# Kernel tuning notes

Measured on AMD Instinct MI355X. Metric: run time of the kernel, lower is better.

The kernel has to match this reference:

```python
import jax, jax.numpy as jnp
import numpy as np

VOC, EDIM, HDIM, SSZ, SDIM, SDEPTH, PAD = 32000, 256, 256, 128, 128, 2, 0
N, BSZ = 64, 32
T = 2 * N - 1  # 127
N_ACTS = 2  # push, pop


def _linear(key, out_d, in_d):
    k1, k2 = jax.random.split(key)
    return (jax.random.normal(k1, (out_d, in_d), jnp.float32) * 0.02,
            jax.random.normal(k2, (out_d,), jnp.float32) * 0.02)


def setup_inputs() -> dict:
    key = jax.random.key(0)
    ks = jax.random.split(key, 9)
    emb_W = jax.random.normal(ks[0], (VOC, EDIM), jnp.float32) * 0.02
    emb_W = emb_W.at[PAD].set(0.0)  # padding_idx row is zero in torch
    W_e2h, b_e2h = _linear(ks[1], HDIM, EDIM)
    W_s2h, b_s2h = _linear(ks[2], HDIM, SDIM * SDEPTH)
    W_h2h, b_h2h = _linear(ks[3], HDIM, HDIM)
    W_h2i, b_h2i = _linear(ks[4], N_ACTS + 1, HDIM)
    W_h2s, b_h2s = _linear(ks[5], SDIM, HDIM)
    W_s2u, b_s2u = _linear(ks[6], SDIM, SDIM * SDEPTH)
    empty_elem = jax.random.normal(ks[7], (1, SDIM), jnp.float32) * 0.02
    inputs = jax.random.randint(ks[8], (N, BSZ), 0, VOC)
    return dict(inputs=inputs, emb_W=emb_W, W_e2h=W_e2h, b_e2h=b_e2h,
                W_s2h=W_s2h, b_s2h=b_s2h, W_h2h=W_h2h, b_h2h=b_h2h,
                W_h2i=W_h2i, b_h2i=b_h2i, W_h2s=W_h2s, b_h2s=b_h2s,
                W_s2u=W_s2u, b_s2u=b_s2u, empty_elem=empty_elem)


def _srnn(inputs, emb_W, W_e2h, b_e2h, W_s2h, b_s2h, W_h2h, b_h2h,
          W_h2i, b_h2i, W_h2s, b_h2s, W_s2u, b_s2u, empty_elem):
    bsz = inputs.shape[1]
    embs = emb_W[inputs]                                        # [N, bsz, edim]
    pads = jnp.broadcast_to(emb_W[PAD], (T - N, bsz, EDIM))     # padded tail
    buf0 = jnp.concatenate([embs, pads], axis=0)                # [T, bsz, edim]
    hid0 = jnp.zeros((bsz, HDIM), jnp.float32)
    stack0 = jnp.broadcast_to(empty_elem, (bsz, SSZ, SDIM))

    def step(carry, t):
        hid, stack, buf = carry
        tops = stack[:, :SDEPTH, :].reshape(bsz, SDEPTH * SDIM)
        inp = buf[t]                                            # [bsz, edim]
        ihid = inp @ W_e2h.T + b_e2h + tops @ W_s2h.T + b_s2h
        hid = jax.nn.relu(hid @ W_h2h.T + b_h2h + ihid)
        inst = ihid @ W_h2i.T + b_h2i                           # [bsz, 3]
        act = jax.nn.softmax(inst[:, :N_ACTS], axis=-1)
        gamma = 1.0 + jnp.log1p(jnp.exp(inst[:, N_ACTS:]))      # [bsz, 1]
        a = act ** gamma
        a = a / (jnp.sum(a, axis=-1, keepdims=True) + 1e-16)    # sharpened acts
        p_push, p_pop = a[:, :1], a[:, 1:]                      # [bsz, 1]
        # buffer update: pop shifts the whole buffer down one slot along time
        buf_pop = jnp.concatenate([jnp.zeros_like(buf[:1]), buf[:-1]], axis=0)
        buf = p_push[None] * buf + p_pop[None] * buf_pop        # [1,bsz,1] bcast
        push_val = jax.nn.relu(hid @ W_h2s.T + b_h2s)           # [bsz, sdim]
        u_val = jax.nn.relu(tops @ W_s2u.T + b_s2u)             # [bsz, sdim]
        z = jnp.zeros((bsz, 1, SDIM), jnp.float32)
        # W_push (shift down by 1) as an index roll
        stack_push = jnp.concatenate([z, stack[:, :-1, :]], axis=1)
        stack_push = stack_push.at[:, 0, :].add(push_val)
        # W_pop = shift up by SDEPTH, then W_push = shift down by 1
        up = jnp.concatenate([stack[:, SDEPTH:, :],
                              jnp.zeros((bsz, SDEPTH, SDIM), jnp.float32)], axis=1)
        stack_pop = jnp.concatenate([z, up[:, :-1, :]], axis=1)
        stack_pop = stack_pop.at[:, 0, :].add(u_val)
        stack_pop = stack_pop.at[:, SSZ - SDEPTH + 1:, :].add(empty_elem[0])
        stack = p_push[:, :, None] * stack_push + p_pop[:, :, None] * stack_pop
        return (hid, stack, buf), (hid, a, stack[:, 0, :])

    (hid, stack, _), (outputs, acts, top_elems) = jax.lax.scan(
        step, (hid0, stack0, buf0), jnp.arange(T))
    return outputs, hid, stack, acts, top_elems


def reference(inputs, emb_W, W_e2h, b_e2h, W_s2h, b_s2h, W_h2h, b_h2h,
              W_h2i, b_h2i, W_h2s, b_h2s, W_s2u, b_s2u, empty_elem):
    return _srnn(inputs, emb_W, W_e2h, b_e2h, W_s2h, b_s2h, W_h2h, b_h2h,
                 W_h2i, b_h2i, W_h2s, b_h2s, W_s2u, b_s2u, empty_elem)
```

## Files before the change

kernel.cpp:

```cpp
#include <hip/hip_runtime.h>
#include <stdint.h>
#include <math.h>


#define T_STEPS 127

#define OUT_OFF   0
#define HID_OFF   1040384
#define STACK_OFF 1048576
#define ACTS_OFF  1572864
#define TE_OFF    1580992

#define WB_OFF 16384
#define E2H_OFF_U 131072

typedef _Float16 h2 __attribute__((ext_vector_type(2)));

__device__ __forceinline__ unsigned packh2(float a, float b){
  h2 v; v.x = (_Float16)a; v.y = (_Float16)b;
  return __builtin_bit_cast(unsigned, v);
}
__device__ __forceinline__ float h2loF(unsigned u){ h2 v = __builtin_bit_cast(h2,u); return (float)v.x; }
__device__ __forceinline__ float h2hiF(unsigned u){ h2 v = __builtin_bit_cast(h2,u); return (float)v.y; }

#if __has_builtin(__builtin_amdgcn_fdot2)
__device__ __forceinline__ float fdot2(unsigned a, unsigned b, float c){
  return __builtin_amdgcn_fdot2(__builtin_bit_cast(h2,a), __builtin_bit_cast(h2,b), c, false);
}
#else
__device__ __forceinline__ float fdot2(unsigned a, unsigned b, float c){
  return c + h2loF(a)*h2loF(b) + h2hiF(a)*h2hiF(b);
}
#endif

#if __has_builtin(__builtin_amdgcn_exp2f)
#define EXP2F(x) __builtin_amdgcn_exp2f(x)
#else
#define EXP2F(x) exp2f(x)
#endif
#if __has_builtin(__builtin_amdgcn_logf)
#define LOG2F(x) __builtin_amdgcn_logf(x)
#else
#define LOG2F(x) log2f(x)
#endif
#if __has_builtin(__builtin_amdgcn_rcpf)
#define RCPF(x) __builtin_amdgcn_rcpf(x)
#else
#define RCPF(x) (1.f/(x))
#endif

#define DPP_XOR1 0xB1
#define DPP_XOR2 0x4E
#define DPP_HM   0x141
#define DPP_RM   0x140
template<int CTRL>
__device__ __forceinline__ float dppadd(float v){
  int s = __builtin_amdgcn_update_dpp(0, __builtin_bit_cast(int, v), CTRL, 0xF, 0xF, true);
  return v + __builtin_bit_cast(float, s);
}

#define BAR() asm volatile("s_waitcnt lgkmcnt(0)\n\ts_barrier" ::: "memory")

#define CHOFF(u) (12*((u)>>3) + ((u)&7))

__global__ void prep_all(const int* __restrict__ inputs, const float* __restrict__ embW,
                         const float* __restrict__ We2h,
                         const float* __restrict__ Ws2h, const float* __restrict__ Wh2h,
                         const float* __restrict__ Wh2s, const float* __restrict__ Ws2u,
                         uint4* __restrict__ out4, unsigned* __restrict__ e2hpk){
  int tid = threadIdx.x;
  int bi  = blockIdx.x;
  if (bi >= 256){
    int gid = (bi-256)*256 + tid;
    const float* src;
    if (gid < 16384){
      int i = gid >> 10, t_ = gid & 1023;
      const float* S = (t_ < 512) ? Ws2h : Wh2h;
      int r = t_ & 511, jp = r >> 2, ks = r & 3;
      int j = 2*jp + (i >> 3);
      int k0 = ks*64 + (i & 7)*8;
      src = S + j*256 + k0;
    } else {
      int l = gid - 16384;
      int i = l >> 10, t_ = l & 1023;
      const float* S = (t_ < 512) ? Wh2s : Ws2u;
      int tt = t_ & 511;
      int j  = 2*(tt >> 3) + (i >> 2);
      int k0 = (tt & 7)*32 + (i & 3)*8;
      src = S + j*256 + k0;
    }
    uint4 r4;
    r4.x = packh2(src[0], src[1]); r4.y = packh2(src[2], src[3]);
    r4.z = packh2(src[4], src[5]); r4.w = packh2(src[6], src[7]);
    out4[gid] = r4;
    return;
  }
  __shared__ float emb[8][256];
  int r2 = bi >> 3, bg = bi & 7;
  for (int q=0;q<8;q++){
    int rr = q >> 2, bb = q & 3;
    int tok = inputs[(2*r2+rr)*32 + bg*4+bb];
    emb[q][tid] = embW[tok*256 + tid];
  }
  __syncthreads();
  float acc[8] = {0.f,0.f,0.f,0.f,0.f,0.f,0.f,0.f};
  for (int i8=0;i8<32;i8++){
    float4 f0 = *(const float4*)&We2h[tid*256 + i8*8];
    float4 f1 = *(const float4*)&We2h[tid*256 + i8*8 + 4];
    float wv[8] = {f0.x,f0.y,f0.z,f0.w,f1.x,f1.y,f1.z,f1.w};
    #pragma unroll
    for (int c=0;c<4;c++){
      float lo = wv[2*c], hi = wv[2*c+1];
      int k = i8*8 + c*2;
      #pragma unroll
      for (int q=0;q<8;q++)
        acc[q] += emb[q][k]*lo + emb[q][k+1]*hi;
    }
  }
  int base = (bg*4)*8192 + r2*256 + tid;
  #pragma unroll
  for (int bb=0;bb<4;bb++)
    e2hpk[base + bb*8192] = packh2(acc[bb], acc[4+bb]);
}

#define GEMV_B(SRC, Y0, Y1) \
  { const uint4* cA0_ = (const uint4*)((SRC) + 24*kB); \
    uint4 A0_ = cA0_[0], A1_ = cA0_[1]; \
    const uint4* cA1_ = (const uint4*)((SRC) + 24*kB + 12); \
    uint4 A2_ = cA1_[0], A3_ = cA1_[1]; \
    Y0=fdot2(A0_.x,wBr[0].x,Y0); Y0=fdot2(A0_.y,wBr[0].y,Y0); Y0=fdot2(A0_.z,wBr[0].z,Y0); Y0=fdot2(A0_.w,wBr[0].w,Y0); \
    Y0=fdot2(A1_.x,wBr[1].x,Y0); Y0=fdot2(A1_.y,wBr[1].y,Y0); Y0=fdot2(A1_.z,wBr[1].z,Y0); Y0=fdot2(A1_.w,wBr[1].w,Y0); \
    Y0=fdot2(A2_.x,wBr[2].x,Y0); Y0=fdot2(A2_.y,wBr[2].y,Y0); Y0=fdot2(A2_.z,wBr[2].z,Y0); Y0=fdot2(A2_.w,wBr[2].w,Y0); \
    Y0=fdot2(A3_.x,wBr[3].x,Y0); Y0=fdot2(A3_.y,wBr[3].y,Y0); Y0=fdot2(A3_.z,wBr[3].z,Y0); Y0=fdot2(A3_.w,wBr[3].w,Y0); \
    Y1=fdot2(A0_.x,wBr[4].x,Y1); Y1=fdot2(A0_.y,wBr[4].y,Y1); Y1=fdot2(A0_.z,wBr[4].z,Y1); Y1=fdot2(A0_.w,wBr[4].w,Y1); \
    Y1=fdot2(A1_.x,wBr[5].x,Y1); Y1=fdot2(A1_.y,wBr[5].y,Y1); Y1=fdot2(A1_.z,wBr[5].z,Y1); Y1=fdot2(A1_.w,wBr[5].w,Y1); \
    Y1=fdot2(A2_.x,wBr[6].x,Y1); Y1=fdot2(A2_.y,wBr[6].y,Y1); Y1=fdot2(A2_.z,wBr[6].z,Y1); Y1=fdot2(A2_.w,wBr[6].w,Y1); \
    Y1=fdot2(A3_.x,wBr[7].x,Y1); Y1=fdot2(A3_.y,wBr[7].y,Y1); Y1=fdot2(A3_.z,wBr[7].z,Y1); Y1=fdot2(A3_.w,wBr[7].w,Y1); \
    Y0 = dppadd<DPP_XOR1>(Y0); Y0 = dppadd<DPP_XOR2>(Y0); Y0 = dppadd<DPP_HM>(Y0); \
    Y1 = dppadd<DPP_XOR1>(Y1); Y1 = dppadd<DPP_XOR2>(Y1); Y1 = dppadd<DPP_HM>(Y1); }

__global__ __attribute__((amdgpu_flat_work_group_size(1024,1024), amdgpu_waves_per_eu(4,4)))
void srnn_main(const uint4* __restrict__ ws4, const unsigned* __restrict__ wsu,
               const float* __restrict__ b_e2h, const float* __restrict__ b_s2h,
               const float* __restrict__ b_h2h, const float* __restrict__ Wh2i,
               const float* __restrict__ b_h2i, const float* __restrict__ b_h2s,
               const float* __restrict__ b_s2u, const float* __restrict__ empty_el,
               float* __restrict__ out)
{
  __shared__ __align__(16) float    stk_s[128*128];
  __shared__ __align__(16) unsigned e2h_s[32*258];
  __shared__ __align__(16) float    halo_top[2][16*128];
  __shared__ __align__(16) float    halo_bot[2][16*128];
  __shared__ __align__(16) unsigned s_pk[192];
  __shared__ __align__(16) unsigned hid_pk[192];
  __shared__ __align__(16) float    pv_s[128], uv_s[128];
  __shared__ __align__(16) float    accih[256], acchp[256];
  __shared__ __align__(16) float    emptyf_s[128];
  __shared__ __align__(16) float    whi_s[768];
  __shared__ __align__(16) float    wbuf[2][192];
  __shared__ __align__(16) unsigned pkwc[32];
  __shared__ float    pp_s, pq_s;

  const int tid = threadIdx.x;
  const int b   = blockIdx.x;
  const int aside = tid >> 9;
  const int ar  = tid & 511;
  const int ajp = ar >> 2;
  const int aks = ar & 3;
  const int pB  = tid >> 3;
  const int kB  = tid & 7;
  const int g   = tid >> 6;
  const int cp  = tid & 63;
  const int sub = (tid >> 5) & 1;
  const int c4  = tid & 31;

  uint4 w1r[16], wBr[8];
  #pragma unroll
  for (int i=0;i<16;i++) w1r[i] = ws4[i*1024 + tid];
  #pragma unroll
  for (int i=0;i<8;i++)  wBr[i] = ws4[WB_OFF + i*1024 + tid];

  float bA0=0.f, bA1=0.f;
  if (aks==0){
    int j0 = 2*ajp;
    if (aside==0){ bA0 = b_e2h[j0]+b_s2h[j0]; bA1 = b_e2h[j0+1]+b_s2h[j0+1]; }
    else         { bA0 = b_h2h[j0];           bA1 = b_h2h[j0+1]; }
  }
  float bB0=0.f, bB1=0.f;
  if (kB==0){
    if (pB < 64){ bB0 = b_h2s[2*pB];      bB1 = b_h2s[2*pB+1]; }
    else        { bB0 = b_s2u[2*(pB-64)]; bB1 = b_s2u[2*(pB-64)+1]; }
  }
  const float bi0=b_h2i[0], bi1=b_h2i[1], bi2=b_h2i[2];

  const unsigned* e2hg = wsu + E2H_OFF_U + b*8192;
  #pragma unroll
  for (int q=0;q<8;q++){
    int idx = q*1024 + tid;
    e2h_s[(idx>>8)*258 + (idx&255)] = e2hg[idx];
  }
  {
    float2 e2 = *(const float2*)&empty_el[2*cp];
    #pragma unroll
    for (int j=0;j<8;j++)
      *(float2*)&stk_s[(8*g+j)*128 + 2*cp] = e2;
    *(float2*)&halo_top[0][g*128 + 2*cp] = e2;
    *(float2*)&halo_bot[0][g*128 + 2*cp] = e2;
    *(float2*)&halo_top[1][g*128 + 2*cp] = e2;
    *(float2*)&halo_bot[1][g*128 + 2*cp] = e2;
  }
  if (tid < 128){
    emptyf_s[tid] = empty_el[tid];
    hid_pk[CHOFF(tid)] = 0u;
    int cu = tid & 63;
    s_pk[CHOFF(tid)] = packh2(empty_el[2*cu], empty_el[2*cu+1]);
  }
  if (tid < 768) whi_s[tid] = Wh2i[tid];
  if (tid < 192){ wbuf[0][tid] = (tid==64)?1.f:0.f; wbuf[1][tid]=0.f; }
  if (tid < 32)  pkwc[tid] = (tid==0)? packh2(1.f,0.f) : 0u;
  __syncthreads();

  int cur = 0;
  for (int t=0;t<T_STEPS;++t){
    {
      const unsigned* act  = aside ? hid_pk : s_pk;
      const unsigned* actB = act + 48*aks;
      float x0 = 0.f, x1 = 0.f;
      if (aside==0){
        uint4 cwa = *(const uint4*)&pkwc[8*aks];
        uint4 cwb = *(const uint4*)&pkwc[8*aks+4];
        unsigned cwv[8] = {cwa.x,cwa.y,cwa.z,cwa.w,cwb.x,cwb.y,cwb.z,cwb.w};
        #pragma unroll
        for (int q=0;q<8;q++){
          int r2 = aks*8 + q;
          unsigned cw = cwv[q];
          uint2 e = *(const uint2*)&e2h_s[r2*258 + 2*ajp];
          x0 = fdot2(cw, e.x, x0);
          x1 = fdot2(cw, e.y, x1);
        }
      }
      #pragma unroll
      for (int i=0;i<8;i++){
        uint4 A  = *(const uint4*)(actB + 12*(i>>1) + 4*(i&1));
        uint4 Wa = w1r[i], Wb = w1r[8+i];
        x0 = fdot2(A.x,Wa.x,x0); x0 = fdot2(A.y,Wa.y,x0);
        x0 = fdot2(A.z,Wa.z,x0); x0 = fdot2(A.w,Wa.w,x0);
        x1 = fdot2(A.x,Wb.x,x1); x1 = fdot2(A.y,Wb.y,x1);
        x1 = fdot2(A.z,Wb.z,x1); x1 = fdot2(A.w,Wb.w,x1);
      }
      x0 = dppadd<DPP_XOR1>(x0); x0 = dppadd<DPP_XOR2>(x0);
      x1 = dppadd<DPP_XOR1>(x1); x1 = dppadd<DPP_XOR2>(x1);
      if (aks==0){
        float* dst = aside ? acchp : accih;
        *(float2*)&dst[2*ajp] = make_float2(x0 + bA0, x1 + bA1);
      }
    }
    BAR();

    if (tid < 64){
      float4 av = *(const float4*)&accih[4*tid];
      float4 q0 = *(const float4*)&whi_s[      4*tid];
      float4 q1 = *(const float4*)&whi_s[256 + 4*tid];
      float4 q2 = *(const float4*)&whi_s[512 + 4*tid];
      float p0 = av.x*q0.x + av.y*q0.y + av.z*q0.z + av.w*q0.w;
      float p1 = av.x*q1.x + av.y*q1.y + av.z*q1.z + av.w*q1.w;
      float p2 = av.x*q2.x + av.y*q2.y + av.z*q2.z + av.w*q2.w;
      p0 = dppadd<DPP_XOR1>(p0); p0 = dppadd<DPP_XOR2>(p0);
      p0 = dppadd<DPP_HM>(p0);   p0 = dppadd<DPP_RM>(p0);
      p1 = dppadd<DPP_XOR1>(p1); p1 = dppadd<DPP_XOR2>(p1);
      p1 = dppadd<DPP_HM>(p1);   p1 = dppadd<DPP_RM>(p1);
      p2 = dppadd<DPP_XOR1>(p2); p2 = dppadd<DPP_XOR2>(p2);
      p2 = dppadd<DPP_HM>(p2);   p2 = dppadd<DPP_RM>(p2);
      p0 += __shfl_xor(p0,16); p0 += __shfl_xor(p0,32);
      p1 += __shfl_xor(p1,16); p1 += __shfl_xor(p1,32);
      p2 += __shfl_xor(p2,16); p2 += __shfl_xor(p2,32);
      if (tid==0){
        float i0 = bi0+p0, i1 = bi1+p1, gi = bi2+p2;
        float gamma = 1.f + 0.6931471806f*LOG2F(1.f + EXP2F(1.442695041f*gi));
        float z = 1.442695041f*gamma*(i0 - i1);
        float ppv = RCPF(1.f + EXP2F(-z));
        float pqv = 1.f - ppv;
        pp_s = ppv; pq_s = pqv;
        *(float2*)&out[ACTS_OFF + t*64 + b*2] = make_float2(ppv,pqv);
      }
    } else if (tid < 192){
      int hl = tid - 64;
      float2 ih2 = *(const float2*)&accih[2*hl];
      float2 hp2 = *(const float2*)&acchp[2*hl];
      float hn0 = fmaxf(ih2.x+hp2.x, 0.f);
      float hn1 = fmaxf(ih2.y+hp2.y, 0.f);
      hid_pk[CHOFF(hl)] = packh2(hn0,hn1);
      *(float2*)&out[OUT_OFF + t*8192 + b*256 + 2*hl] = make_float2(hn0,hn1);
      if (t==T_STEPS-1) *(float2*)&out[HID_OFF + b*256 + 2*hl] = make_float2(hn0,hn1);
    }
    if (tid >= 512){
      float y0=0.f, y1=0.f;
      GEMV_B(s_pk, y0, y1);
      if (kB==0){
        *(float2*)&uv_s[2*(pB-64)] =
          make_float2(fmaxf(y0+bB0,0.f), fmaxf(y1+bB1,0.f));
      }
    }
    BAR();

    if (tid < 512){
      float y0=0.f, y1=0.f;
      GEMV_B(hid_pk, y0, y1);
      if (kB==0){
        *(float2*)&pv_s[2*pB] =
          make_float2(fmaxf(y0+bB0,0.f), fmaxf(y1+bB1,0.f));
      }
    }
    BAR();
    const float pp = pp_s, pq = pq_s;

    if (tid < 128){
      int k = 64+tid;
      wbuf[cur^1][k] = pp*wbuf[cur][k] + pq*wbuf[cur][k-1];
    } else if (tid < 160){
      int r2 = tid-128;
      int k1 = 65 + t - 2*r2;
      float wa = wbuf[cur][k1], wb2 = wbuf[cur][k1-1], wc2 = wbuf[cur][k1-2];
      pkwc[r2] = packh2(pp*wa+pq*wb2, pp*wb2+pq*wc2);
    }

    {
      const int R = 8*g + 4*sub;
      if (R <= t){
        float4 o0, o1, o2, o3, o4, o5;
        o1 = *(const float4*)&stk_s[(R  )*128 + 4*c4];
        o2 = *(const float4*)&stk_s[(R+1)*128 + 4*c4];
        o3 = *(const float4*)&stk_s[(R+2)*128 + 4*c4];
        o4 = *(const float4*)&stk_s[(R+3)*128 + 4*c4];
        if (sub == 0){
          o0 = (g>0) ? *(const float4*)&halo_bot[cur][(g-1)*128 + 4*c4]
                     : make_float4(0.f,0.f,0.f,0.f);
          o5 = *(const float4*)&stk_s[(R+4)*128 + 4*c4];
        } else {
          o0 = *(const float4*)&stk_s[(R-1)*128 + 4*c4];
          o5 = (g<15) ? *(const float4*)&halo_top[cur][(g+1)*128 + 4*c4]
                      : *(const float4*)&emptyf_s[4*c4];
        }
        float4 n0, n1, n2, n3;
        n0.x = pp*o0.x + pq*o2.x; n0.y = pp*o0.y + pq*o2.y;
        n0.z = pp*o0.z + pq*o2.z; n0.w = pp*o0.w + pq*o2.w;
        n1.x = pp*o1.x + pq*o3.x; n1.y = pp*o1.y + pq*o3.y;
        n1.z = pp*o1.z + pq*o3.z; n1.w = pp*o1.w + pq*o3.w;
        n2.x = pp*o2.x + pq*o4.x; n2.y = pp*o2.y + pq*o4.y;
        n2.z = pp*o2.z + pq*o4.z; n2.w = pp*o2.w + pq*o4.w;
        n3.x = pp*o3.x + pq*o5.x; n3.y = pp*o3.y + pq*o5.y;
        n3.z = pp*o3.z + pq*o5.z; n3.w = pp*o3.w + pq*o5.w;
        if (g == 0 && sub == 0){
          float4 pv4 = *(const float4*)&pv_s[4*c4];
          float4 uv4 = *(const float4*)&uv_s[4*c4];
          n0.x = pp*pv4.x + pq*uv4.x; n0.y = pp*pv4.y + pq*uv4.y;
          n0.z = pp*pv4.z + pq*uv4.z; n0.w = pp*pv4.w + pq*uv4.w;
        }
        *(float4*)&stk_s[(R  )*128 + 4*c4] = n0;
        *(float4*)&stk_s[(R+1)*128 + 4*c4] = n1;
        *(float4*)&stk_s[(R+2)*128 + 4*c4] = n2;
        *(float4*)&stk_s[(R+3)*128 + 4*c4] = n3;
        if (sub == 0) *(float4*)&halo_top[cur^1][g*128 + 4*c4] = n0;
        else          *(float4*)&halo_bot[cur^1][g*128 + 4*c4] = n3;
        if (g == 0 && sub == 0){
          *(float4*)&out[TE_OFF + t*4096 + b*128 + 4*c4] = n0;
          s_pk[CHOFF(2*c4)]      = packh2(n0.x, n0.y);
          s_pk[CHOFF(2*c4+1)]    = packh2(n0.z, n0.w);
          s_pk[CHOFF(64+2*c4)]   = packh2(n1.x, n1.y);
          s_pk[CHOFF(64+2*c4+1)] = packh2(n1.z, n1.w);
        }
      }
    }
    BAR();
    cur ^= 1;
  }

  {
    const int R = 8*g + 4*sub;
    #pragma unroll
    for (int j=0;j<4;j++){
      *(float4*)&out[STACK_OFF + b*16384 + (R+j)*128 + 4*c4] =
        *(const float4*)&stk_s[(R+j)*128 + 4*c4];
    }
  }
}

extern "C" void kernel_launch(void* const* d_in, const int* in_sizes, int n_in,
                              void* d_out, int out_size, void* d_ws, size_t ws_size,
                              hipStream_t stream){
  const int*   inputs = (const int*)d_in[0];
  const float* embW   = (const float*)d_in[1];
  const float* We2h   = (const float*)d_in[2];
  const float* b_e2h  = (const float*)d_in[3];
  const float* Ws2h   = (const float*)d_in[4];
  const float* b_s2h  = (const float*)d_in[5];
  const float* Wh2h   = (const float*)d_in[6];
  const float* b_h2h  = (const float*)d_in[7];
  const float* Wh2i   = (const float*)d_in[8];
  const float* b_h2i  = (const float*)d_in[9];
  const float* Wh2s   = (const float*)d_in[10];
  const float* b_h2s  = (const float*)d_in[11];
  const float* Ws2u   = (const float*)d_in[12];
  const float* b_s2u  = (const float*)d_in[13];
  const float* empty  = (const float*)d_in[14];
  unsigned* wsu = (unsigned*)d_ws;

  prep_all<<<dim3(352), dim3(256), 0, stream>>>(inputs, embW, We2h, Ws2h, Wh2h,
                                                Wh2s, Ws2u, (uint4*)wsu,
                                                wsu + E2H_OFF_U);
  srnn_main<<<dim3(32), dim3(1024), 0, stream>>>((const uint4*)wsu, (const unsigned*)wsu,
                                                 b_e2h, b_s2h, b_h2h, Wh2i, b_h2i,
                                                 b_h2s, b_s2u, empty, (float*)d_out);
}
```

Measured before the change: 803.0 us.

## Overlap stack update with push-value GEMV across thread halves

The stack mixing update, previously a separate phase after all GEMVs, is split. The upper half of threads updates its stack rows while the lower half computes the push-value GEMV, and the lower half updates its rows after the next barrier. To make the split uniform, the R<=t row-skipping guard is dropped, so every row is updated every step. That removes a serialized phase per timestep but adds redundant work on untouched rows in early steps, and it relies on the g==0 rows (which need pv_s) belonging to the lower half.

```diff
diff --git a/kernel.cpp b/kernel.cpp
--- a/kernel.cpp
+++ b/kernel.cpp
@@ -139,6 +139,52 @@
     Y0 = dppadd<DPP_XOR1>(Y0); Y0 = dppadd<DPP_XOR2>(Y0); Y0 = dppadd<DPP_HM>(Y0); \
     Y1 = dppadd<DPP_XOR1>(Y1); Y1 = dppadd<DPP_XOR2>(Y1); Y1 = dppadd<DPP_HM>(Y1); }
 
+#define STACK_UPDATE() do { \
+  const int R_ = 8*g + 4*sub; \
+  float4 o0, o1, o2, o3, o4, o5; \
+  o1 = *(const float4*)&stk_s[(R_  )*128 + 4*c4]; \
+  o2 = *(const float4*)&stk_s[(R_+1)*128 + 4*c4]; \
+  o3 = *(const float4*)&stk_s[(R_+2)*128 + 4*c4]; \
+  o4 = *(const float4*)&stk_s[(R_+3)*128 + 4*c4]; \
+  if (sub == 0){ \
+    o0 = (g>0) ? *(const float4*)&halo_bot[cur][(g-1)*128 + 4*c4] \
+               : make_float4(0.f,0.f,0.f,0.f); \
+    o5 = *(const float4*)&stk_s[(R_+4)*128 + 4*c4]; \
+  } else { \
+    o0 = *(const float4*)&stk_s[(R_-1)*128 + 4*c4]; \
+    o5 = (g<15) ? *(const float4*)&halo_top[cur][(g+1)*128 + 4*c4] \
+                : *(const float4*)&emptyf_s[4*c4]; \
+  } \
+  float4 n0, n1, n2, n3; \
+  n0.x = pp*o0.x + pq*o2.x; n0.y = pp*o0.y + pq*o2.y; \
+  n0.z = pp*o0.z + pq*o2.z; n0.w = pp*o0.w + pq*o2.w; \
+  n1.x = pp*o1.x + pq*o3.x; n1.y = pp*o1.y + pq*o3.y; \
+  n1.z = pp*o1.z + pq*o3.z; n1.w = pp*o1.w + pq*o3.w; \
+  n2.x = pp*o2.x + pq*o4.x; n2.y = pp*o2.y + pq*o4.y; \
+  n2.z = pp*o2.z + pq*o4.z; n2.w = pp*o2.w + pq*o4.w; \
+  n3.x = pp*o3.x + pq*o5.x; n3.y = pp*o3.y + pq*o5.y; \
+  n3.z = pp*o3.z + pq*o5.z; n3.w = pp*o3.w + pq*o5.w; \
+  if (g == 0 && sub == 0){ \
+    float4 pv4 = *(const float4*)&pv_s[4*c4]; \
+    float4 uv4 = *(const float4*)&uv_s[4*c4]; \
+    n0.x = pp*pv4.x + pq*uv4.x; n0.y = pp*pv4.y + pq*uv4.y; \
+    n0.z = pp*pv4.z + pq*uv4.z; n0.w = pp*pv4.w + pq*uv4.w; \
+  } \
+  *(float4*)&stk_s[(R_  )*128 + 4*c4] = n0; \
+  *(float4*)&stk_s[(R_+1)*128 + 4*c4] = n1; \
+  *(float4*)&stk_s[(R_+2)*128 + 4*c4] = n2; \
+  *(float4*)&stk_s[(R_+3)*128 + 4*c4] = n3; \
+  if (sub == 0) *(float4*)&halo_top[cur^1][g*128 + 4*c4] = n0;   \
+  else          *(float4*)&halo_bot[cur^1][g*128 + 4*c4] = n3;   \
+  if (g == 0 && sub == 0){ \
+    *(float4*)&out[TE_OFF + t*4096 + b*128 + 4*c4] = n0; \
+    s_pk[CHOFF(2*c4)]      = packh2(n0.x, n0.y); \
+    s_pk[CHOFF(2*c4+1)]    = packh2(n0.z, n0.w); \
+    s_pk[CHOFF(64+2*c4)]   = packh2(n1.x, n1.y); \
+    s_pk[CHOFF(64+2*c4+1)] = packh2(n1.z, n1.w); \
+  } \
+} while(0)
+
 __global__ __attribute__((amdgpu_flat_work_group_size(1024,1024), amdgpu_waves_per_eu(4,4)))
 void srnn_main(const uint4* __restrict__ ws4, const unsigned* __restrict__ wsu,
                const float* __restrict__ b_e2h, const float* __restrict__ b_s2h,
@@ -206,8 +252,6 @@
       *(float2*)&stk_s[(8*g+j)*128 + 2*cp] = e2;
     *(float2*)&halo_top[0][g*128 + 2*cp] = e2;
     *(float2*)&halo_bot[0][g*128 + 2*cp] = e2;
-    *(float2*)&halo_top[1][g*128 + 2*cp] = e2;
-    *(float2*)&halo_bot[1][g*128 + 2*cp] = e2;
   }
   if (tid < 128){
     emptyf_s[tid] = empty_el[tid];
@@ -302,6 +346,7 @@
       }
     }
     BAR();
+    const float pp = pp_s, pq = pq_s;
 
     if (tid < 512){
       float y0=0.f, y1=0.f;
@@ -310,10 +355,14 @@
         *(float2*)&pv_s[2*pB] =
           make_float2(fmaxf(y0+bB0,0.f), fmaxf(y1+bB1,0.f));
       }
+    } else {
+      STACK_UPDATE();
     }
     BAR();
-    const float pp = pp_s, pq = pq_s;
-
+
+    if (tid < 512){
+      STACK_UPDATE();
+    }
     if (tid < 128){
       int k = 64+tid;
       wbuf[cur^1][k] = pp*wbuf[cur][k] + pq*wbuf[cur][k-1];
@@ -322,54 +371,6 @@
       int k1 = 65 + t - 2*r2;
       float wa = wbuf[cur][k1], wb2 = wbuf[cur][k1-1], wc2 = wbuf[cur][k1-2];
       pkwc[r2] = packh2(pp*wa+pq*wb2, pp*wb2+pq*wc2);
-    }
-
-    {
-      const int R = 8*g + 4*sub;
-      if (R <= t){
-        float4 o0, o1, o2, o3, o4, o5;
-        o1 = *(const float4*)&stk_s[(R  )*128 + 4*c4];
-        o2 = *(const float4*)&stk_s[(R+1)*128 + 4*c4];
-        o3 = *(const float4*)&stk_s[(R+2)*128 + 4*c4];
-        o4 = *(const float4*)&stk_s[(R+3)*128 + 4*c4];
-        if (sub == 0){
-          o0 = (g>0) ? *(const float4*)&halo_bot[cur][(g-1)*128 + 4*c4]
-                     : make_float4(0.f,0.f,0.f,0.f);
-          o5 = *(const float4*)&stk_s[(R+4)*128 + 4*c4];
-        } else {
-          o0 = *(const float4*)&stk_s[(R-1)*128 + 4*c4];
-          o5 = (g<15) ? *(const float4*)&halo_top[cur][(g+1)*128 + 4*c4]
-                      : *(const float4*)&emptyf_s[4*c4];
-        }
-        float4 n0, n1, n2, n3;
-        n0.x = pp*o0.x + pq*o2.x; n0.y = pp*o0.y + pq*o2.y;
-        n0.z = pp*o0.z + pq*o2.z; n0.w = pp*o0.w + pq*o2.w;
-        n1.x = pp*o1.x + pq*o3.x; n1.y = pp*o1.y + pq*o3.y;
-        n1.z = pp*o1.z + pq*o3.z; n1.w = pp*o1.w + pq*o3.w;
-        n2.x = pp*o2.x + pq*o4.x; n2.y = pp*o2.y + pq*o4.y;
-        n2.z = pp*o2.z + pq*o4.z; n2.w = pp*o2.w + pq*o4.w;
-        n3.x = pp*o3.x + pq*o5.x; n3.y = pp*o3.y + pq*o5.y;
-        n3.z = pp*o3.z + pq*o5.z; n3.w = pp*o3.w + pq*o5.w;
-        if (g == 0 && sub == 0){
-          float4 pv4 = *(const float4*)&pv_s[4*c4];
-          float4 uv4 = *(const float4*)&uv_s[4*c4];
-          n0.x = pp*pv4.x + pq*uv4.x; n0.y = pp*pv4.y + pq*uv4.y;
-          n0.z = pp*pv4.z + pq*uv4.z; n0.w = pp*pv4.w + pq*uv4.w;
-        }
-        *(float4*)&stk_s[(R  )*128 + 4*c4] = n0;
-        *(float4*)&stk_s[(R+1)*128 + 4*c4] = n1;
-        *(float4*)&stk_s[(R+2)*128 + 4*c4] = n2;
-        *(float4*)&stk_s[(R+3)*128 + 4*c4] = n3;
-        if (sub == 0) *(float4*)&halo_top[cur^1][g*128 + 4*c4] = n0;
-        else          *(float4*)&halo_bot[cur^1][g*128 + 4*c4] = n3;
-        if (g == 0 && sub == 0){
-          *(float4*)&out[TE_OFF + t*4096 + b*128 + 4*c4] = n0;
-          s_pk[CHOFF(2*c4)]      = packh2(n0.x, n0.y);
-          s_pk[CHOFF(2*c4+1)]    = packh2(n0.z, n0.w);
-          s_pk[CHOFF(64+2*c4)]   = packh2(n1.x, n1.y);
-          s_pk[CHOFF(64+2*c4+1)] = packh2(n1.z, n1.w);
-        }
-      }
     }
     BAR();
     cur ^= 1;
```

After: 792.3 us. No clear change (-1.3%).

## Overlap hidden-state GEMV with stack update phase across thread halves

Applied to the files above, without the earlier changes.

Moves the W_h2h·hid GEMV, computed by threads 512+, out of the first phase of each step and into the stack-update phase of the previous step, so it runs alongside the stack shift done by threads below 512. The first phase now only computes the input/stack projection, and acchp is initialized with the bias before the loop. The stack update also drops its R<=t guard and always updates every row, which removes a branch but does extra work on rows that are still empty. The aim is to shorten the critical path per time step, at the cost of a more intricate cross-step dependency on hid_pk.

```diff
diff --git a/kernel.cpp b/kernel.cpp
--- a/kernel.cpp
+++ b/kernel.cpp
@@ -206,8 +206,6 @@
       *(float2*)&stk_s[(8*g+j)*128 + 2*cp] = e2;
     *(float2*)&halo_top[0][g*128 + 2*cp] = e2;
     *(float2*)&halo_bot[0][g*128 + 2*cp] = e2;
-    *(float2*)&halo_top[1][g*128 + 2*cp] = e2;
-    *(float2*)&halo_bot[1][g*128 + 2*cp] = e2;
   }
   if (tid < 128){
     emptyf_s[tid] = empty_el[tid];
@@ -218,15 +216,16 @@
   if (tid < 768) whi_s[tid] = Wh2i[tid];
   if (tid < 192){ wbuf[0][tid] = (tid==64)?1.f:0.f; wbuf[1][tid]=0.f; }
   if (tid < 32)  pkwc[tid] = (tid==0)? packh2(1.f,0.f) : 0u;
+  if (tid >= 512 && aks == 0)
+    *(float2*)&acchp[2*ajp] = make_float2(bA0, bA1);
   __syncthreads();
 
   int cur = 0;
   for (int t=0;t<T_STEPS;++t){
-    {
-      const unsigned* act  = aside ? hid_pk : s_pk;
-      const unsigned* actB = act + 48*aks;
+    if (tid < 512){
+      const unsigned* actB = s_pk + 48*aks;
       float x0 = 0.f, x1 = 0.f;
-      if (aside==0){
+      {
         uint4 cwa = *(const uint4*)&pkwc[8*aks];
         uint4 cwb = *(const uint4*)&pkwc[8*aks+4];
         unsigned cwv[8] = {cwa.x,cwa.y,cwa.z,cwa.w,cwb.x,cwb.y,cwb.z,cwb.w};
@@ -251,8 +250,7 @@
       x0 = dppadd<DPP_XOR1>(x0); x0 = dppadd<DPP_XOR2>(x0);
       x1 = dppadd<DPP_XOR1>(x1); x1 = dppadd<DPP_XOR2>(x1);
       if (aks==0){
-        float* dst = aside ? acchp : accih;
-        *(float2*)&dst[2*ajp] = make_float2(x0 + bA0, x1 + bA1);
+        *(float2*)&accih[2*ajp] = make_float2(x0 + bA0, x1 + bA1);
       }
     }
     BAR();
@@ -314,61 +312,76 @@
     BAR();
     const float pp = pp_s, pq = pq_s;
 
-    if (tid < 128){
-      int k = 64+tid;
-      wbuf[cur^1][k] = pp*wbuf[cur][k] + pq*wbuf[cur][k-1];
-    } else if (tid < 160){
-      int r2 = tid-128;
-      int k1 = 65 + t - 2*r2;
-      float wa = wbuf[cur][k1], wb2 = wbuf[cur][k1-1], wc2 = wbuf[cur][k1-2];
-      pkwc[r2] = packh2(pp*wa+pq*wb2, pp*wb2+pq*wc2);
-    }
-
     {
       const int R = 8*g + 4*sub;
-      if (R <= t){
-        float4 o0, o1, o2, o3, o4, o5;
-        o1 = *(const float4*)&stk_s[(R  )*128 + 4*c4];
-        o2 = *(const float4*)&stk_s[(R+1)*128 + 4*c4];
-        o3 = *(const float4*)&stk_s[(R+2)*128 + 4*c4];
-        o4 = *(const float4*)&stk_s[(R+3)*128 + 4*c4];
-        if (sub == 0){
-          o0 = (g>0) ? *(const float4*)&halo_bot[cur][(g-1)*128 + 4*c4]
-                     : make_float4(0.f,0.f,0.f,0.f);
-          o5 = *(const float4*)&stk_s[(R+4)*128 + 4*c4];
-        } else {
-          o0 = *(const float4*)&stk_s[(R-1)*128 + 4*c4];
-          o5 = (g<15) ? *(const float4*)&halo_top[cur][(g+1)*128 + 4*c4]
-                      : *(const float4*)&emptyf_s[4*c4];
-        }
-        float4 n0, n1, n2, n3;
-        n0.x = pp*o0.x + pq*o2.x; n0.y = pp*o0.y + pq*o2.y;
-        n0.z = pp*o0.z + pq*o2.z; n0.w = pp*o0.w + pq*o2.w;
-        n1.x = pp*o1.x + pq*o3.x; n1.y = pp*o1.y + pq*o3.y;
-        n1.z = pp*o1.z + pq*o3.z; n1.w = pp*o1.w + pq*o3.w;
-        n2.x = pp*o2.x + pq*o4.x; n2.y = pp*o2.y + pq*o4.y;
-        n2.z = pp*o2.z + pq*o4.z; n2.w = pp*o2.w + pq*o4.w;
-        n3.x = pp*o3.x + pq*o5.x; n3.y = pp*o3.y + pq*o5.y;
-        n3.z = pp*o3.z + pq*o5.z; n3.w = pp*o3.w + pq*o5.w;
-        if (g == 0 && sub == 0){
-          float4 pv4 = *(const float4*)&pv_s[4*c4];
-          float4 uv4 = *(const float4*)&uv_s[4*c4];
-          n0.x = pp*pv4.x + pq*uv4.x; n0.y = pp*pv4.y + pq*uv4.y;
-          n0.z = pp*pv4.z + pq*uv4.z; n0.w = pp*pv4.w + pq*uv4.w;
-        }
-        *(float4*)&stk_s[(R  )*128 + 4*c4] = n0;
-        *(float4*)&stk_s[(R+1)*128 + 4*c4] = n1;
-        *(float4*)&stk_s[(R+2)*128 + 4*c4] = n2;
-        *(float4*)&stk_s[(R+3)*128 + 4*c4] = n3;
-        if (sub == 0) *(float4*)&halo_top[cur^1][g*128 + 4*c4] = n0;
-        else          *(float4*)&halo_bot[cur^1][g*128 + 4*c4] = n3;
-        if (g == 0 && sub == 0){
-          *(float4*)&out[TE_OFF + t*4096 + b*128 + 4*c4] = n0;
-          s_pk[CHOFF(2*c4)]      = packh2(n0.x, n0.y);
-          s_pk[CHOFF(2*c4+1)]    = packh2(n0.z, n0.w);
-          s_pk[CHOFF(64+2*c4)]   = packh2(n1.x, n1.y);
-          s_pk[CHOFF(64+2*c4+1)] = packh2(n1.z, n1.w);
-        }
+      float4 o0, o1, o2, o3, o4, o5;
+      o1 = *(const float4*)&stk_s[(R  )*128 + 4*c4];
+      o2 = *(const float4*)&stk_s[(R+1)*128 + 4*c4];
+      o3 = *(const float4*)&stk_s[(R+2)*128 + 4*c4];
+      o4 = *(const float4*)&stk_s[(R+3)*128 + 4*c4];
+      if (sub == 0){
+        o0 = (g>0) ? *(const float4*)&halo_bot[cur][(g-1)*128 + 4*c4]
+                   : make_float4(0.f,0.f,0.f,0.f);
+        o5 = *(const float4*)&stk_s[(R+4)*128 + 4*c4];
+      } else {
+        o0 = *(const float4*)&stk_s[(R-1)*128 + 4*c4];
+        o5 = (g<15) ? *(const float4*)&halo_top[cur][(g+1)*128 + 4*c4]
+                    : *(const float4*)&emptyf_s[4*c4];
+      }
+      float4 n0, n1, n2, n3;
+      n0.x = pp*o0.x + pq*o2.x; n0.y = pp*o0.y + pq*o2.y;
+      n0.z = pp*o0.z + pq*o2.z; n0.w = pp*o0.w + pq*o2.w;
+      n1.x = pp*o1.x + pq*o3.x; n1.y = pp*o1.y + pq*o3.y;
+      n1.z = pp*o1.z + pq*o3.z; n1.w = pp*o1.w + pq*o3.w;
+      n2.x = pp*o2.x + pq*o4.x; n2.y = pp*o2.y + pq*o4.y;
+      n2.z = pp*o2.z + pq*o4.z; n2.w = pp*o2.w + pq*o4.w;
+      n3.x = pp*o3.x + pq*o5.x; n3.y = pp*o3.y + pq*o5.y;
+      n3.z = pp*o3.z + pq*o5.z; n3.w = pp*o3.w + pq*o5.w;
+      if (g == 0 && sub == 0){
+        float4 pv4 = *(const float4*)&pv_s[4*c4];
+        float4 uv4 = *(const float4*)&uv_s[4*c4];
+        n0.x = pp*pv4.x + pq*uv4.x; n0.y = pp*pv4.y + pq*uv4.y;
+        n0.z = pp*pv4.z + pq*uv4.z; n0.w = pp*pv4.w + pq*uv4.w;
+      }
+      *(float4*)&stk_s[(R  )*128 + 4*c4] = n0;
+      *(float4*)&stk_s[(R+1)*128 + 4*c4] = n1;
+      *(float4*)&stk_s[(R+2)*128 + 4*c4] = n2;
+      *(float4*)&stk_s[(R+3)*128 + 4*c4] = n3;
+      if (sub == 0) *(float4*)&halo_top[cur^1][g*128 + 4*c4] = n0;
+      else          *(float4*)&halo_bot[cur^1][g*128 + 4*c4] = n3;
+      if (g == 0 && sub == 0){
+        *(float4*)&out[TE_OFF + t*4096 + b*128 + 4*c4] = n0;
+        s_pk[CHOFF(2*c4)]      = packh2(n0.x, n0.y);
+        s_pk[CHOFF(2*c4+1)]    = packh2(n0.z, n0.w);
+        s_pk[CHOFF(64+2*c4)]   = packh2(n1.x, n1.y);
+        s_pk[CHOFF(64+2*c4+1)] = packh2(n1.z, n1.w);
+      }
+      if (tid < 128){
+        int k = 64+tid;
+        wbuf[cur^1][k] = pp*wbuf[cur][k] + pq*wbuf[cur][k-1];
+      } else if (tid < 160){
+        int r2 = tid-128;
+        int k1 = 65 + t - 2*r2;
+        float wa = wbuf[cur][k1], wb2 = wbuf[cur][k1-1], wc2 = wbuf[cur][k1-2];
+        pkwc[r2] = packh2(pp*wa+pq*wb2, pp*wb2+pq*wc2);
+      }
+    }
+    if (tid >= 512){
+      const unsigned* actB = hid_pk + 48*aks;
+      float x0 = 0.f, x1 = 0.f;
+      #pragma unroll
+      for (int i=0;i<8;i++){
+        uint4 A  = *(const uint4*)(actB + 12*(i>>1) + 4*(i&1));
+        uint4 Wa = w1r[i], Wb = w1r[8+i];
+        x0 = fdot2(A.x,Wa.x,x0); x0 = fdot2(A.y,Wa.y,x0);
+        x0 = fdot2(A.z,Wa.z,x0); x0 = fdot2(A.w,Wa.w,x0);
+        x1 = fdot2(A.x,Wb.x,x1); x1 = fdot2(A.y,Wb.y,x1);
+        x1 = fdot2(A.z,Wb.z,x1); x1 = fdot2(A.w,Wb.w,x1);
+      }
+      x0 = dppadd<DPP_XOR1>(x0); x0 = dppadd<DPP_XOR2>(x0);
+      x1 = dppadd<DPP_XOR1>(x1); x1 = dppadd<DPP_XOR2>(x1);
+      if (aks==0){
+        *(float2*)&acchp[2*ajp] = make_float2(x0 + bA0, x1 + bA1);
       }
     }
     BAR();
```

New measurement: 758.7 us. -5.5%, faster.
